# Performance work log

Measured on AMD Instinct MI355X. Metric: run time of the kernel, lower is better.

Reference implementation:

```python
import jax, jax.numpy as jnp
import numpy as np

B, C, L = 32, 64, 4096
HIDDEN = 64
SR = 50.0
KS = (7, 15, 31, 63)
PHYS = 12
EPS_BN = 1e-5
EPS_GN = 1e-5


def _dwconv(x, w):
    # x: (B,C,L), w: (C,1,k) depthwise kernel, SAME padding for odd k
    k = w.shape[-1]
    p = (k - 1) // 2
    return jax.lax.conv_general_dilated(
        x, w, window_strides=(1,), padding=[(p, p)],
        dimension_numbers=('NCH', 'OIH', 'NCH'),
        feature_group_count=x.shape[1])


def _physics(x):
    b, c, l = x.shape
    svm = jnp.sqrt((x * x).sum(axis=1))                      # (B,L) channel norm
    svm_max = svm.max(axis=-1)
    svm_mean = svm.mean(axis=-1)
    svm_std = jnp.std(svm, axis=-1, ddof=1) + 1e-6           # torch.std is unbiased
    jerk = jnp.diff(x, axis=-1) * SR                         # (B,C,L-1)
    jerk_max = jnp.abs(jerk).max(axis=-1).mean(axis=-1)      # (B,)
    jerk_rate = jnp.diff(jerk, axis=-1) * SR
    jerk_rate_max = jnp.abs(jerk_rate).max(axis=-1).mean(axis=-1)
    sign_changes = (x[:, :, :-1] * x[:, :, 1:] < 0).astype(x.dtype)
    zcr = sign_changes.sum(axis=-1).mean(axis=-1) / l
    thr = (svm_mean + 2.0 * svm_std)[:, None]
    impact_duration = (svm > thr).astype(x.dtype).sum(axis=-1) / l
    hthr = (svm_mean + 3.0 * svm_std)[:, None]
    impact_ratio = (svm > hthr).astype(x.dtype).sum(axis=-1) / l
    free_fall = (svm < (svm_mean - svm_std)[:, None]).astype(x.dtype).sum(axis=-1) / l
    second_half = svm[:, l // 2:]
    post_stillness = jnp.tanh(1.0 / (jnp.std(second_half, axis=-1, ddof=1) + 1e-6))
    third = max(1, l // 3)
    pre_mean = svm[:, :third].mean(axis=-1)
    impact_peak = svm[:, third:2 * third].max(axis=-1)
    post_mean = svm[:, 2 * third:].mean(axis=-1)
    fall_phase = jax.nn.relu(impact_peak - pre_mean) + jax.nn.relu(impact_peak - post_mean)
    fall_phase = fall_phase / (jnp.abs(impact_peak) + 1e-6)
    spectrum = jnp.fft.rfft(x.astype(jnp.float32), axis=-1, norm='ortho')
    power = (jnp.abs(spectrum) ** 2).sum(axis=1)             # (B, L//2+1)
    freqs = jnp.linspace(0.0, 1.0, power.shape[-1], dtype=power.dtype)
    total_power = power.sum(axis=-1) + 1e-6
    spectral_centroid = (power * freqs).sum(axis=-1) / total_power
    high_freq_ratio = jnp.where(freqs > 0.4, power, 0.0).sum(axis=-1) / total_power
    feats = jnp.stack([svm_max, svm_mean, jerk_max, jerk_rate_max, zcr,
                       impact_duration, impact_ratio, post_stillness, free_fall,
                       spectral_centroid, high_freq_ratio, fall_phase], axis=-1)
    return jnp.nan_to_num(feats, nan=0.0, posinf=0.0, neginf=0.0).astype(x.dtype)


def _forward(x, dw_w7, dw_w15, dw_w31, dw_w63, bn_g, bn_b, bn_m, bn_v,
             comp_w1, comp_b1, comp_w2, comp_b2,
             pn_g, pn_b, pn_m, pn_v,
             pe_w1, pe_b1, pe_w2, pe_b2, pg_w, pg_b,
             temperature, gn_g, gn_b, proj_w, proj_b, res_scale):
    # 4 depthwise conv + BN(eval) branches
    branches = []
    for i, w in enumerate((dw_w7, dw_w15, dw_w31, dw_w63)):
        y = _dwconv(x, w)
        y = (y - bn_m[i][None, :, None]) / jnp.sqrt(bn_v[i][None, :, None] + EPS_BN) \
            * bn_g[i][None, :, None] + bn_b[i][None, :, None]
        branches.append(y)
    stacked = jnp.stack(branches, axis=1)                    # (B,4,C,L)
    # complexity net: global avg pool -> MLP
    xm = x.mean(axis=-1)                                     # (B,C)
    h = jax.nn.relu(xm @ comp_w1 + comp_b1)
    complexity_logits = h @ comp_w2 + comp_b2                # (B,4)
    # physics gate
    pf = _physics(x)                                         # (B,12)
    pf = (pf - pn_m) / jnp.sqrt(pn_v + EPS_BN) * pn_g + pn_b
    pe = jax.nn.relu(jax.nn.relu(pf @ pe_w1 + pe_b1) @ pe_w2 + pe_b2)
    physics_weights = jax.nn.sigmoid(pe @ pg_w + pg_b)       # (B,4)
    temp = jnp.maximum(temperature, 0.1)
    weights = jax.nn.softmax(complexity_logits * physics_weights / temp, axis=-1)
    mixed = jnp.einsum('bkcl,bk->bcl', stacked, weights)
    # proj: GroupNorm(1,C) -> GELU(exact) -> 1x1 conv
    mu = mixed.mean(axis=(1, 2), keepdims=True)
    var = mixed.var(axis=(1, 2), keepdims=True)
    gn = (mixed - mu) / jnp.sqrt(var + EPS_GN) * gn_g[None, :, None] + gn_b[None, :, None]
    act = jax.nn.gelu(gn, approximate=False)
    out = jnp.einsum('oc,bcl->bol', proj_w, act) + proj_b[None, :, None]
    return x + res_scale * out


def setup_inputs() -> dict:
    ks = jax.random.split(jax.random.key(0), 16)
    f32 = jnp.float32
    inp = {}
    inp['x'] = jax.random.normal(ks[0], (B, C, L), dtype=f32)
    for i, k in enumerate(KS):
        inp[f'dw_w{k}'] = jax.random.normal(ks[1 + i], (C, 1, k), dtype=f32) / np.sqrt(k)
    inp['bn_g'] = jnp.ones((4, C), f32)
    inp['bn_b'] = jnp.zeros((4, C), f32)
    inp['bn_m'] = 0.1 * jax.random.normal(ks[5], (4, C), dtype=f32)
    inp['bn_v'] = jax.random.uniform(ks[6], (4, C), dtype=f32, minval=0.5, maxval=1.5)
    inp['comp_w1'] = jax.random.normal(ks[7], (C, HIDDEN), dtype=f32) / np.sqrt(C)
    inp['comp_b1'] = jnp.zeros((HIDDEN,), f32)
    inp['comp_w2'] = jax.random.normal(ks[8], (HIDDEN, 4), dtype=f32) / np.sqrt(HIDDEN)
    inp['comp_b2'] = jnp.zeros((4,), f32)
    inp['pn_g'] = jnp.ones((PHYS,), f32)
    inp['pn_b'] = jnp.zeros((PHYS,), f32)
    inp['pn_m'] = 0.1 * jax.random.normal(ks[9], (PHYS,), dtype=f32)
    inp['pn_v'] = jax.random.uniform(ks[10], (PHYS,), dtype=f32, minval=0.5, maxval=1.5)
    inp['pe_w1'] = jax.random.normal(ks[11], (PHYS, 32), dtype=f32) / np.sqrt(PHYS)
    inp['pe_b1'] = jnp.zeros((32,), f32)
    inp['pe_w2'] = jax.random.normal(ks[12], (32, 32), dtype=f32) / np.sqrt(32)
    inp['pe_b2'] = jnp.zeros((32,), f32)
    inp['pg_w'] = jax.random.normal(ks[13], (32, 4), dtype=f32) / np.sqrt(32)
    inp['pg_b'] = jnp.zeros((4,), f32)
    inp['temperature'] = jnp.asarray(1.0, f32)
    inp['gn_g'] = jnp.ones((C,), f32)
    inp['gn_b'] = jnp.zeros((C,), f32)
    inp['proj_w'] = jax.random.normal(ks[14], (C, C), dtype=f32) / np.sqrt(C)
    inp['proj_b'] = jnp.zeros((C,), f32)
    inp['res_scale'] = jnp.asarray(0.5, f32)  # init is 0.0; 0.5 gives a non-trivial output
    return inp


def reference(x, dw_w7, dw_w15, dw_w31, dw_w63, bn_g, bn_b, bn_m, bn_v,
              comp_w1, comp_b1, comp_w2, comp_b2,
              pn_g, pn_b, pn_m, pn_v,
              pe_w1, pe_b1, pe_w2, pe_b2, pg_w, pg_b,
              temperature, gn_g, gn_b, proj_w, proj_b, res_scale):
    return _forward(x, dw_w7, dw_w15, dw_w31, dw_w63, bn_g, bn_b, bn_m, bn_v,
                    comp_w1, comp_b1, comp_w2, comp_b2, pn_g, pn_b, pn_m, pn_v,
                    pe_w1, pe_b1, pe_w2, pe_b2, pg_w, pg_b,
                    temperature, gn_g, gn_b, proj_w, proj_b, res_scale)
```

## Files before the change

kernel.cpp:

```cpp
#include <hip/hip_runtime.h>
#include <math.h>

#define LN 4096
#define CN 64
#define BQ 32
#define NTH 256

#define OFF_CHAN_SUM    0
#define OFF_CHAN_JERK   2048
#define OFF_CHAN_JRATE  4096
#define OFF_CHAN_ZCR    6144
#define OFF_SVMST_PART  8192
#define OFF_SPEC_PART   12288
#define OFF_EFF_B       15360
#define OFF_GNP         17408
#define OFF_EFF_W       21504
#define OFF_SVMBUF      152576

#define FP(i) ((i) + ((i) >> 4))

__global__ __launch_bounds__(NTH) void kS(const float* __restrict__ x, float* __restrict__ ws) {
  __shared__ __align__(16) char smraw[34880];
  int role = blockIdx.x;
  int t = threadIdx.x;

  if (role < 2048) {
    int bc = role;
    const float* row = x + (size_t)bc * LN;
    int l0 = t * 16;
    float rd[18];
    const float4* r4 = (const float4*)(row + l0);
#pragma unroll
    for (int q = 0; q < 4; q++) {
      float4 v = r4[q];
      rd[4*q] = v.x; rd[4*q+1] = v.y; rd[4*q+2] = v.z; rd[4*q+3] = v.w;
    }
    if (t < 255) { rd[16] = row[l0 + 16]; rd[17] = row[l0 + 17]; }
    else { rd[16] = 0.f; rd[17] = 0.f; }
    float lsum = 0.f, jm = 0.f, jrm = 0.f; int zc = 0;
#pragma unroll
    for (int i = 0; i < 16; i++) {
      float a = rd[i], b2 = rd[i+1];
      lsum += a;
      int l = l0 + i;
      if (l < LN - 1) {
        jm = fmaxf(jm, fabsf(b2 - a));
        zc += (a * b2 < 0.f);
        if (l < LN - 2) jrm = fmaxf(jrm, fabsf(rd[i+2] - 2.f*b2 + a));
      }
    }
    for (int off = 32; off > 0; off >>= 1) {
      lsum += __shfl_down(lsum, off);
      jm = fmaxf(jm, __shfl_down(jm, off));
      jrm = fmaxf(jrm, __shfl_down(jrm, off));
      zc += __shfl_down(zc, off);
    }
    float* s1 = (float*)smraw; float* s2_ = s1 + 4; float* s3 = s1 + 8; int* s4 = (int*)(s1 + 12);
    int w = t >> 6;
    if ((t & 63) == 0) { s1[w] = lsum; s2_[w] = jm; s3[w] = jrm; s4[w] = zc; }
    __syncthreads();
    if (t == 0) {
      float S = 0, J = 0, JR = 0; int Z = 0;
      for (int i = 0; i < 4; i++) { S += s1[i]; J = fmaxf(J, s2_[i]); JR = fmaxf(JR, s3[i]); Z += s4[i]; }
      ws[OFF_CHAN_SUM + bc]   = S;
      ws[OFF_CHAN_JERK + bc]  = J * 50.f;
      ws[OFF_CHAN_JRATE + bc] = JR * 2500.f;
      ws[OFF_CHAN_ZCR + bc]   = (float)Z;
    }
  } else if (role < 2560) {
    int blk = role - 2048;
    int b = blk >> 4, lt = blk & 15;
    int l = lt * 256 + t;
    const float* xb = x + (size_t)b * CN * LN + l;
    float acc = 0.f;
#pragma unroll
    for (int c = 0; c < CN; c++) { float v = xb[(size_t)c * LN]; acc = fmaf(v, v, acc); }
    float svm = sqrtf(acc);
    ws[OFF_SVMBUF + (size_t)b * LN + l] = svm;
    const int third = LN / 3;
    float vS = svm, vS2 = svm * svm;
    float vS2H  = (l >= LN/2) ? svm : 0.f;
    float vS2H2 = (l >= LN/2) ? svm * svm : 0.f;
    float vPRE  = (l < third) ? svm : 0.f;
    float vPOST = (l >= 2*third) ? svm : 0.f;
    float vMX = svm;
    float vMID = (l >= third && l < 2*third) ? svm : 0.f;
    for (int off = 32; off > 0; off >>= 1) {
      vS += __shfl_down(vS, off); vS2 += __shfl_down(vS2, off);
      vS2H += __shfl_down(vS2H, off); vS2H2 += __shfl_down(vS2H2, off);
      vPRE += __shfl_down(vPRE, off); vPOST += __shfl_down(vPOST, off);
      vMX = fmaxf(vMX, __shfl_down(vMX, off));
      vMID = fmaxf(vMID, __shfl_down(vMID, off));
    }
    float (*red)[4] = (float(*)[4])smraw;
    int w = t >> 6;
    if ((t & 63) == 0) {
      red[0][w] = vS; red[1][w] = vS2; red[2][w] = vMX; red[3][w] = vS2H;
      red[4][w] = vS2H2; red[5][w] = vPRE; red[6][w] = vMID; red[7][w] = vPOST;
    }
    __syncthreads();
    if (t == 0) {
      float* sp = ws + OFF_SVMST_PART + (size_t)blk * 8;
      sp[0] = red[0][0]+red[0][1]+red[0][2]+red[0][3];
      sp[1] = red[1][0]+red[1][1]+red[1][2]+red[1][3];
      sp[2] = fmaxf(fmaxf(red[2][0],red[2][1]),fmaxf(red[2][2],red[2][3]));
      sp[3] = red[3][0]+red[3][1]+red[3][2]+red[3][3];
      sp[4] = red[4][0]+red[4][1]+red[4][2]+red[4][3];
      sp[5] = red[5][0]+red[5][1]+red[5][2]+red[5][3];
      sp[6] = fmaxf(fmaxf(red[6][0],red[6][1]),fmaxf(red[6][2],red[6][3]));
      sp[7] = red[7][0]+red[7][1]+red[7][2]+red[7][3];
    }
  } else {
    int blk = role - 2560;
    int b = blk >> 5, cp = blk & 31;
    const float* r0 = x + ((size_t)b * CN + 2 * cp) * LN;
    const float* r1 = r0 + LN;
    float2* z = (float2*)smraw;
    float (*red)[4] = (float(*)[4])(smraw + 34816);
#pragma unroll
    for (int k = 0; k < 4; k++) {
      int n4 = (k * 256 + t) * 4;
      float4 a = *(const float4*)(r0 + n4);
      float4 c = *(const float4*)(r1 + n4);
      float ar[4] = {a.x, a.y, a.z, a.w}, cr[4] = {c.x, c.y, c.z, c.w};
#pragma unroll
      for (int q = 0; q < 4; q++) {
        unsigned n = (unsigned)(n4 + q);
        unsigned br = __brev(n) >> 20;
        unsigned dr = ((br & 0x555u) << 1) | ((br & 0xAAAu) >> 1);
        z[FP(dr)] = make_float2(ar[q], cr[q]);
      }
    }
    __syncthreads();
#pragma unroll
    for (int u = 0; u < 4; u++) {
      int j = u * 256 + t;
      int i0 = 4 * j;
      float2 x0 = z[FP(i0)], x1 = z[FP(i0+1)], x2 = z[FP(i0+2)], x3 = z[FP(i0+3)];
      float ar = x0.x + x2.x, ai = x0.y + x2.y;
      float br_ = x0.x - x2.x, bi = x0.y - x2.y;
      float cr = x1.x + x3.x, ci = x1.y + x3.y;
      float dr_ = x1.x - x3.x, di = x1.y - x3.y;
      z[FP(i0)]   = make_float2(ar + cr, ai + ci);
      z[FP(i0+1)] = make_float2(br_ + di, bi - dr_);
      z[FP(i0+2)] = make_float2(ar - cr, ai - ci);
      z[FP(i0+3)] = make_float2(br_ - di, bi + dr_);
    }
    __syncthreads();
#pragma unroll
    for (int s = 1; s < 6; s++) {
      int half = 1 << (2 * s);
      float angscale = 1.0f / (float)(2 * half);
#pragma unroll
      for (int u = 0; u < 4; u++) {
        int j = u * 256 + t;
        int pos = j & (half - 1);
        int i0 = ((j >> (2 * s)) << (2 * s + 2)) + pos;
        float2 x0 = z[FP(i0)];
        float2 x1 = z[FP(i0 + half)];
        float2 x2 = z[FP(i0 + 2 * half)];
        float2 x3 = z[FP(i0 + 3 * half)];
        float sv, cv;
        sincospif((float)pos * angscale, &sv, &cv);
        float w1r = cv, w1i = -sv;
        float w2r = w1r*w1r - w1i*w1i, w2i = 2.f*w1r*w1i;
        float w3r = w2r*w1r - w2i*w1i, w3i = w2r*w1i + w2i*w1r;
        float t1r = x1.x*w1r - x1.y*w1i, t1i = x1.x*w1i + x1.y*w1r;
        float t2r = x2.x*w2r - x2.y*w2i, t2i = x2.x*w2i + x2.y*w2r;
        float t3r = x3.x*w3r - x3.y*w3i, t3i = x3.x*w3i + x3.y*w3r;
        float ar = x0.x + t2r, ai = x0.y + t2i;
        float br_ = x0.x - t2r, bi = x0.y - t2i;
        float cr = t1r + t3r, ci = t1i + t3i;
        float dr_ = t1r - t3r, di = t1i - t3i;
        z[FP(i0)]            = make_float2(ar + cr, ai + ci);
        z[FP(i0 + half)]     = make_float2(br_ + di, bi - dr_);
        z[FP(i0 + 2*half)]   = make_float2(ar - cr, ai - ci);
        z[FP(i0 + 3*half)]   = make_float2(br_ - di, bi + dr_);
      }
      __syncthreads();
    }
    float tot = 0.f, cen = 0.f, hi = 0.f;
    for (int k = t; k <= LN / 2; k += NTH) {
      float p;
      if (k == 0 || k == LN / 2) {
        float2 v = z[FP(k)];
        p = v.x * v.x + v.y * v.y;
      } else {
        float2 zk = z[FP(k)], zn = z[FP(LN - k)];
        float a1 = zk.x + zn.x, a2 = zk.y - zn.y, a3 = zk.y + zn.y, a4 = zk.x - zn.x;
        p = 0.25f * (a1*a1 + a2*a2 + a3*a3 + a4*a4);
      }
      p *= (1.0f / LN);
      tot += p;
      cen += p * ((float)k * (1.0f / (LN / 2)));
      if (k >= 820) hi += p;
    }
    for (int off = 32; off > 0; off >>= 1) {
      tot += __shfl_down(tot, off);
      cen += __shfl_down(cen, off);
      hi  += __shfl_down(hi, off);
    }
    int w = t >> 6;
    if ((t & 63) == 0) { red[0][w] = tot; red[1][w] = cen; red[2][w] = hi; }
    __syncthreads();
    if (t == 0) {
      float* sp = ws + OFF_SPEC_PART + (size_t)blk * 3;
      sp[0] = red[0][0]+red[0][1]+red[0][2]+red[0][3];
      sp[1] = red[1][0]+red[1][1]+red[1][2]+red[1][3];
      sp[2] = red[2][0]+red[2][1]+red[2][2]+red[2][3];
    }
  }
}

__global__ __launch_bounds__(NTH) void k4_gate(
    const float* __restrict__ dw7, const float* __restrict__ dw15,
    const float* __restrict__ dw31, const float* __restrict__ dw63,
    const float* __restrict__ bn_g, const float* __restrict__ bn_b,
    const float* __restrict__ bn_m, const float* __restrict__ bn_v,
    const float* __restrict__ comp_w1, const float* __restrict__ comp_b1,
    const float* __restrict__ comp_w2, const float* __restrict__ comp_b2,
    const float* __restrict__ pn_g, const float* __restrict__ pn_b,
    const float* __restrict__ pn_m, const float* __restrict__ pn_v,
    const float* __restrict__ pe_w1, const float* __restrict__ pe_b1,
    const float* __restrict__ pe_w2, const float* __restrict__ pe_b2,
    const float* __restrict__ pg_w, const float* __restrict__ pg_b,
    const float* __restrict__ temperature,
    float* __restrict__ ws)
{
  int b = blockIdx.x, t = threadIdx.x;
  __shared__ float sp8[16][8];
  __shared__ float sp3[32][3];
  __shared__ float stv[10];
  __shared__ float bc2[2];
  __shared__ float xm[64], h[64], pf[12], pe1v[32], pe2v[32], lgts[4], wts[4];
  __shared__ int ri[3][4], cnts[3];
  if (t < 16) {
    const float* p = ws + OFF_SVMST_PART + (size_t)(b * 16 + t) * 8;
#pragma unroll
    for (int i = 0; i < 8; i++) sp8[t][i] = p[i];
  }
  if (t >= 32 && t < 64) {
    int i = t - 32;
    const float* p = ws + OFF_SPEC_PART + (size_t)(b * 32 + i) * 3;
    sp3[i][0] = p[0]; sp3[i][1] = p[1]; sp3[i][2] = p[2];
  }
  __syncthreads();
  if (t == 0) {
    float S=0,S2=0,MX=-1e30f,S2H=0,S2H2=0,PRE=0,MID=-1e30f,POST=0;
    for (int i = 0; i < 16; i++) {
      S += sp8[i][0]; S2 += sp8[i][1]; MX = fmaxf(MX, sp8[i][2]);
      S2H += sp8[i][3]; S2H2 += sp8[i][4]; PRE += sp8[i][5];
      MID = fmaxf(MID, sp8[i][6]); POST += sp8[i][7];
    }
    float tot=0,cen=0,hi=0;
    for (int i = 0; i < 32; i++) { tot += sp3[i][0]; cen += sp3[i][1]; hi += sp3[i][2]; }
    stv[0]=S; stv[1]=S2; stv[2]=MX; stv[3]=S2H; stv[4]=S2H2;
    stv[5]=PRE; stv[6]=MID; stv[7]=POST; stv[8]=cen/(tot+1e-6f); stv[9]=hi/(tot+1e-6f);
    float mean = S * (1.f / LN);
    float var = (S2 - S * S * (1.f / LN)) * (1.f / (LN - 1));
    var = fmaxf(var, 0.f);
    bc2[0] = mean;
    bc2[1] = sqrtf(var) + 1e-6f;
  }
  __syncthreads();
  float mean = bc2[0], stde = bc2[1];
  float thr2 = mean + 2.f * stde, thr3 = mean + 3.f * stde, thrf = mean - stde;
  const float* svm = ws + OFF_SVMBUF + (size_t)b * LN;
  int c2 = 0, c3 = 0, cf = 0;
  for (int l = t; l < LN; l += NTH) {
    float v = svm[l];
    c2 += (v > thr2); c3 += (v > thr3); cf += (v < thrf);
  }
  for (int off = 32; off > 0; off >>= 1) {
    c2 += __shfl_down(c2, off); c3 += __shfl_down(c3, off); cf += __shfl_down(cf, off);
  }
  int w = t >> 6;
  if ((t & 63) == 0) { ri[0][w] = c2; ri[1][w] = c3; ri[2][w] = cf; }
  float j = 0.f, jr = 0.f, zz = 0.f;
  if (t < 64) {
    xm[t] = ws[OFF_CHAN_SUM + b * 64 + t] * (1.0f / LN);
    j  = ws[OFF_CHAN_JERK + b * 64 + t];
    jr = ws[OFF_CHAN_JRATE + b * 64 + t];
    zz = ws[OFF_CHAN_ZCR + b * 64 + t];
    for (int off = 32; off > 0; off >>= 1) {
      j += __shfl_down(j, off); jr += __shfl_down(jr, off); zz += __shfl_down(zz, off);
    }
  }
  __syncthreads();
  if (t == 0) {
    cnts[0] = ri[0][0]+ri[0][1]+ri[0][2]+ri[0][3];
    cnts[1] = ri[1][0]+ri[1][1]+ri[1][2]+ri[1][3];
    cnts[2] = ri[2][0]+ri[2][1]+ri[2][2]+ri[2][3];
    const int third = LN / 3;
    float S2H = stv[3], S2H2 = stv[4];
    float n2 = (float)(LN / 2);
    float var2 = (S2H2 - S2H * S2H / n2) / (n2 - 1.f);
    var2 = fmaxf(var2, 0.f);
    float post_still = tanhf(1.f / (sqrtf(var2) + 1e-6f));
    float pre_mean = stv[5] / (float)third;
    float post_mean = stv[7] / (float)(LN - 2 * third);
    float pk = stv[6];
    float fp = fmaxf(pk - pre_mean, 0.f) + fmaxf(pk - post_mean, 0.f);
    fp = fp / (fabsf(pk) + 1e-6f);
    pf[0] = stv[2];
    pf[1] = mean;
    pf[2] = j * (1.f / 64);
    pf[3] = jr * (1.f / 64);
    pf[4] = (zz * (1.f / 64)) * (1.f / LN);
    pf[5] = (float)cnts[0] / LN;
    pf[6] = (float)cnts[1] / LN;
    pf[7] = post_still;
    pf[8] = (float)cnts[2] / LN;
    pf[9] = stv[8];
    pf[10] = stv[9];
    pf[11] = fp;
  }
  __syncthreads();
  if (t < 12) pf[t] = (pf[t] - pn_m[t]) * rsqrtf(pn_v[t] + 1e-5f) * pn_g[t] + pn_b[t];
  __syncthreads();
  if (t < 64) {
    float hv = comp_b1[t];
    for (int i = 0; i < 64; i++) hv = fmaf(xm[i], comp_w1[i * 64 + t], hv);
    h[t] = fmaxf(hv, 0.f);
  }
  if (t < 32) {
    float v = pe_b1[t];
    for (int i = 0; i < 12; i++) v = fmaf(pf[i], pe_w1[i * 32 + t], v);
    pe1v[t] = fmaxf(v, 0.f);
  }
  __syncthreads();
  if (t < 32) {
    float v = pe_b2[t];
    for (int i = 0; i < 32; i++) v = fmaf(pe1v[i], pe_w2[i * 32 + t], v);
    pe2v[t] = fmaxf(v, 0.f);
  }
  __syncthreads();
  if (t < 4) {
    float v = comp_b2[t];
    for (int i = 0; i < 64; i++) v = fmaf(h[i], comp_w2[i * 4 + t], v);
    float g = pg_b[t];
    for (int i = 0; i < 32; i++) g = fmaf(pe2v[i], pg_w[i * 4 + t], g);
    g = 1.f / (1.f + expf(-g));
    float temp = fmaxf(temperature[0], 0.1f);
    lgts[t] = v * g / temp;
  }
  __syncthreads();
  if (t < 4) {
    float m = fmaxf(fmaxf(lgts[0], lgts[1]), fmaxf(lgts[2], lgts[3]));
    float den = expf(lgts[0]-m) + expf(lgts[1]-m) + expf(lgts[2]-m) + expf(lgts[3]-m);
    wts[t] = expf(lgts[t] - m) / den;
  }
  __syncthreads();
  if (t < 64) {
    int c = t;
    float w0 = wts[0], w1 = wts[1], w2 = wts[2], w3 = wts[3];
    float sc0 = bn_g[0*64+c] * rsqrtf(bn_v[0*64+c] + 1e-5f);
    float sc1 = bn_g[1*64+c] * rsqrtf(bn_v[1*64+c] + 1e-5f);
    float sc2 = bn_g[2*64+c] * rsqrtf(bn_v[2*64+c] + 1e-5f);
    float sc3 = bn_g[3*64+c] * rsqrtf(bn_v[3*64+c] + 1e-5f);
    float o0 = bn_b[0*64+c] - bn_m[0*64+c] * sc0;
    float o1 = bn_b[1*64+c] - bn_m[1*64+c] * sc1;
    float o2 = bn_b[2*64+c] - bn_m[2*64+c] * sc2;
    float o3 = bn_b[3*64+c] - bn_m[3*64+c] * sc3;
    ws[OFF_EFF_B + b * 64 + c] = w0*o0 + w1*o1 + w2*o2 + w3*o3;
    float a0 = w0*sc0, a1 = w1*sc1, a2 = w2*sc2, a3 = w3*sc3;
    float* eff = ws + OFF_EFF_W + (size_t)(b * 64 + c) * 64;
    for (int tau = 0; tau < 64; tau++) {
      float v = 0.f;
      if (tau < 63) {
        v = a3 * dw63[c * 63 + tau];
        int i7 = tau - 28;  if (i7 >= 0 && i7 < 7)   v = fmaf(a0, dw7[c * 7 + i7], v);
        int i15 = tau - 24; if (i15 >= 0 && i15 < 15) v = fmaf(a1, dw15[c * 15 + i15], v);
        int i31 = tau - 16; if (i31 >= 0 && i31 < 31) v = fmaf(a2, dw31[c * 31 + i31], v);
      }
      eff[tau] = v;
    }
  }
}

__device__ __forceinline__ float4 ldmask(const float* __restrict__ row, int idx) {
  int idxc = idx < 0 ? 0 : (idx > LN - 4 ? LN - 4 : idx);
  float4 v = *(const float4*)(row + idxc);
  float m = (idx == idxc) ? 1.f : 0.f;
  v.x *= m; v.y *= m; v.z *= m; v.w *= m;
  return v;
}

#define F16(wv,a0,a1,a2,a3,a4,a5,a6,a7,a8,a9,aA,aB,aC,aD,aE,aF) \
  acc[0]=fmaf(wv,a0,acc[0]);  acc[1]=fmaf(wv,a1,acc[1]);  acc[2]=fmaf(wv,a2,acc[2]);  acc[3]=fmaf(wv,a3,acc[3]);  \
  acc[4]=fmaf(wv,a4,acc[4]);  acc[5]=fmaf(wv,a5,acc[5]);  acc[6]=fmaf(wv,a6,acc[6]);  acc[7]=fmaf(wv,a7,acc[7]);  \
  acc[8]=fmaf(wv,a8,acc[8]);  acc[9]=fmaf(wv,a9,acc[9]);  acc[10]=fmaf(wv,aA,acc[10]); acc[11]=fmaf(wv,aB,acc[11]); \
  acc[12]=fmaf(wv,aC,acc[12]); acc[13]=fmaf(wv,aD,acc[13]); acc[14]=fmaf(wv,aE,acc[14]); acc[15]=fmaf(wv,aF,acc[15]);

__global__ __launch_bounds__(NTH) void k5_conv(const float* __restrict__ x,
                                               float* __restrict__ ws,
                                               float* __restrict__ mixed_out) {
  int bc = blockIdx.x;
  int t = threadIdx.x;
  __shared__ float wt[64];
  __shared__ float biasS;
  __shared__ double rda[2][4];
  if (t < 64) wt[t] = ws[OFF_EFF_W + (size_t)bc * 64 + t];
  if (t == 0) biasS = ws[OFF_EFF_B + bc];
  const float* row = x + (size_t)bc * LN;
  int l0 = t * 16;
  int g0 = l0 - 32;
  float4 R0 = ldmask(row, g0);
  float4 R1 = ldmask(row, g0 + 4);
  float4 R2 = ldmask(row, g0 + 8);
  float4 R3 = ldmask(row, g0 + 12);
  float4 R4 = ldmask(row, g0 + 16);
  __syncthreads();
  float bias = biasS;
  float acc[16];
#pragma unroll
  for (int jj = 0; jj < 16; jj++) acc[jj] = bias;
#pragma unroll
  for (int g = 0; g < 16; g++) {
    float w0 = wt[4*g], w1 = wt[4*g+1], w2 = wt[4*g+2], w3 = wt[4*g+3];
    F16(w0, R0.y,R0.z,R0.w,R1.x,R1.y,R1.z,R1.w,R2.x,R2.y,R2.z,R2.w,R3.x,R3.y,R3.z,R3.w,R4.x)
    F16(w1, R0.z,R0.w,R1.x,R1.y,R1.z,R1.w,R2.x,R2.y,R2.z,R2.w,R3.x,R3.y,R3.z,R3.w,R4.x,R4.y)
    F16(w2, R0.w,R1.x,R1.y,R1.z,R1.w,R2.x,R2.y,R2.z,R2.w,R3.x,R3.y,R3.z,R3.w,R4.x,R4.y,R4.z)
    F16(w3, R1.x,R1.y,R1.z,R1.w,R2.x,R2.y,R2.z,R2.w,R3.x,R3.y,R3.z,R3.w,R4.x,R4.y,R4.z,R4.w)
    if (g < 15) {
      R0 = R1; R1 = R2; R2 = R3; R3 = R4;
      R4 = ldmask(row, g0 + 4 * (g + 5));
    }
  }
  double ls = 0, ls2 = 0;
#pragma unroll
  for (int jj = 0; jj < 16; jj++) { float v = acc[jj]; ls += v; ls2 += (double)v * (double)v; }
  for (int off = 32; off > 0; off >>= 1) {
    ls += __shfl_down(ls, off);
    ls2 += __shfl_down(ls2, off);
  }
  int w = t >> 6;
  if ((t & 63) == 0) { rda[0][w] = ls; rda[1][w] = ls2; }
  __syncthreads();
  if (t == 0) {
    double* gp = (double*)(ws + OFF_GNP);
    gp[2 * bc + 0] = rda[0][0]+rda[0][1]+rda[0][2]+rda[0][3];
    gp[2 * bc + 1] = rda[1][0]+rda[1][1]+rda[1][2]+rda[1][3];
  }
  float* dst = mixed_out + (size_t)bc * LN + l0;
#pragma unroll
  for (int q = 0; q < 4; q++) {
    float4 v; v.x = acc[4*q]; v.y = acc[4*q+1]; v.z = acc[4*q+2]; v.w = acc[4*q+3];
    *(float4*)(dst + 4 * q) = v;
  }
}

__global__ __launch_bounds__(NTH) void k6_final(const float* __restrict__ x,
    const float* __restrict__ proj_w, const float* __restrict__ proj_b,
    const float* __restrict__ gn_g, const float* __restrict__ gn_b,
    const float* __restrict__ res_scale,
    const float* __restrict__ ws, float* out) {
  int blk = blockIdx.x;
  int b = blk >> 5;
  int l0 = (blk & 31) * 128;
  __shared__ float actS[64 * 128];
  __shared__ float Wt[64 * 64];
  __shared__ double rg[2][4];
  __shared__ float bcst[2];
  int t = threadIdx.x;
  {
    const double* gp = (const double*)(ws + OFF_GNP) + (size_t)b * CN * 2;
    double s1 = 0, s2 = 0;
    for (int i = t; i < CN; i += NTH) { s1 += gp[2*i]; s2 += gp[2*i+1]; }
    for (int off = 32; off > 0; off >>= 1) { s1 += __shfl_down(s1, off); s2 += __shfl_down(s2, off); }
    int w = t >> 6;
    if ((t & 63) == 0) { rg[0][w] = s1; rg[1][w] = s2; }
    __syncthreads();
    if (t == 0) {
      double S1 = rg[0][0]+rg[0][1]+rg[0][2]+rg[0][3];
      double S2 = rg[1][0]+rg[1][1]+rg[1][2]+rg[1][3];
      const double NN = 64.0 * 4096.0;
      double mud = S1 / NN;
      bcst[0] = (float)mud;
      bcst[1] = rsqrtf((float)(S2 / NN - mud * mud) + 1e-5f);
    }
  }
  for (int i = t; i < 4096; i += NTH) {
    int o = i & 63, c = i >> 6;
    Wt[c * 64 + o] = proj_w[o * 64 + c];
  }
  __syncthreads();
  float mu = bcst[0], rstd = bcst[1];
  const float* mx = out + (size_t)b * CN * LN;
  for (int i = t; i < 8192; i += NTH) {
    int c = i >> 7, l = i & 127;
    float v = mx[(size_t)c * LN + l0 + l];
    float g = (v - mu) * rstd * gn_g[c] + gn_b[c];
    float a = 0.5f * g * (1.f + erff(g * 0.70710678118654752f));
    actS[c * 128 + l] = a;
  }
  __syncthreads();
  int lg = t & 31;
  int og = (t >> 5) * 8;
  float4 acc4[8];
#pragma unroll
  for (int q = 0; q < 8; q++) { acc4[q].x = 0.f; acc4[q].y = 0.f; acc4[q].z = 0.f; acc4[q].w = 0.f; }
  for (int c = 0; c < 64; c++) {
    float4 a = *(const float4*)&actS[c * 128 + lg * 4];
    float4 wlo = *(const float4*)&Wt[c * 64 + og];
    float4 whi = *(const float4*)&Wt[c * 64 + og + 4];
    float wv[8] = { wlo.x, wlo.y, wlo.z, wlo.w, whi.x, whi.y, whi.z, whi.w };
#pragma unroll
    for (int q = 0; q < 8; q++) {
      acc4[q].x = fmaf(wv[q], a.x, acc4[q].x);
      acc4[q].y = fmaf(wv[q], a.y, acc4[q].y);
      acc4[q].z = fmaf(wv[q], a.z, acc4[q].z);
      acc4[q].w = fmaf(wv[q], a.w, acc4[q].w);
    }
  }
  float rsv = res_scale[0];
  const float* xb = x + (size_t)b * CN * LN;
  float* ob = out + (size_t)b * CN * LN;
#pragma unroll
  for (int q = 0; q < 8; q++) {
    int o = og + q;
    float pb = proj_b[o];
    size_t base = (size_t)o * LN + l0 + lg * 4;
    float4 xv = *(const float4*)&xb[base];
    float4 r;
    r.x = xv.x + rsv * (acc4[q].x + pb);
    r.y = xv.y + rsv * (acc4[q].y + pb);
    r.z = xv.z + rsv * (acc4[q].z + pb);
    r.w = xv.w + rsv * (acc4[q].w + pb);
    *(float4*)&ob[base] = r;
  }
}

extern "C" void kernel_launch(void* const* d_in, const int* in_sizes, int n_in,
                              void* d_out, int out_size, void* d_ws, size_t ws_size,
                              hipStream_t stream) {
  const float* x        = (const float*)d_in[0];
  const float* dw7      = (const float*)d_in[1];
  const float* dw15     = (const float*)d_in[2];
  const float* dw31     = (const float*)d_in[3];
  const float* dw63     = (const float*)d_in[4];
  const float* bn_g     = (const float*)d_in[5];
  const float* bn_b     = (const float*)d_in[6];
  const float* bn_m     = (const float*)d_in[7];
  const float* bn_v     = (const float*)d_in[8];
  const float* comp_w1  = (const float*)d_in[9];
  const float* comp_b1  = (const float*)d_in[10];
  const float* comp_w2  = (const float*)d_in[11];
  const float* comp_b2  = (const float*)d_in[12];
  const float* pn_g     = (const float*)d_in[13];
  const float* pn_b     = (const float*)d_in[14];
  const float* pn_m     = (const float*)d_in[15];
  const float* pn_v     = (const float*)d_in[16];
  const float* pe_w1    = (const float*)d_in[17];
  const float* pe_b1    = (const float*)d_in[18];
  const float* pe_w2    = (const float*)d_in[19];
  const float* pe_b2    = (const float*)d_in[20];
  const float* pg_w     = (const float*)d_in[21];
  const float* pg_b     = (const float*)d_in[22];
  const float* temperature = (const float*)d_in[23];
  const float* gn_g     = (const float*)d_in[24];
  const float* gn_b     = (const float*)d_in[25];
  const float* proj_w   = (const float*)d_in[26];
  const float* proj_b   = (const float*)d_in[27];
  const float* res_scale= (const float*)d_in[28];
  float* ws = (float*)d_ws;
  float* out = (float*)d_out;

  hipLaunchKernelGGL(kS, dim3(2048 + 512 + 1024), dim3(NTH), 0, stream, x, ws);
  hipLaunchKernelGGL(k4_gate, dim3(BQ), dim3(NTH), 0, stream,
                     dw7, dw15, dw31, dw63, bn_g, bn_b, bn_m, bn_v,
                     comp_w1, comp_b1, comp_w2, comp_b2,
                     pn_g, pn_b, pn_m, pn_v, pe_w1, pe_b1, pe_w2, pe_b2,
                     pg_w, pg_b, temperature, ws);
  hipLaunchKernelGGL(k5_conv, dim3(BQ * CN), dim3(NTH), 0, stream, x, ws, out);
  hipLaunchKernelGGL(k6_final, dim3(BQ * 32), dim3(NTH), 0, stream,
                     x, proj_w, proj_b, gn_g, gn_b, res_scale, ws, out);
}
```

Baseline: 242.2 us.

## Fuse radix-4 FFT stages into radix-16 register passes

Replaces the six radix-4 FFT stages over shared memory with three passes. In each pass a thread loads 16 elements into registers and applies two radix-4 layers there. This halves the number of shared-memory round trips and barriers in the spectrum computation. The cost is higher register pressure and twiddles built from chained products, which may lose some accuracy.

```diff
diff --git a/kernel.cpp b/kernel.cpp
--- a/kernel.cpp
+++ b/kernel.cpp
@@ -18,6 +18,22 @@
 #define OFF_SVMBUF      152576
 
 #define FP(i) ((i) + ((i) >> 4))
+
+__device__ __forceinline__ void bfly4(float2& a, float2& b, float2& c, float2& d,
+                                      float w1r, float w1i, float w2r, float w2i,
+                                      float w3r, float w3i) {
+  float t1r = b.x*w1r - b.y*w1i, t1i = b.x*w1i + b.y*w1r;
+  float t2r = c.x*w2r - c.y*w2i, t2i = c.x*w2i + c.y*w2r;
+  float t3r = d.x*w3r - d.y*w3i, t3i = d.x*w3i + d.y*w3r;
+  float ar = a.x + t2r, ai = a.y + t2i;
+  float br = a.x - t2r, bi = a.y - t2i;
+  float cr = t1r + t3r, ci = t1i + t3i;
+  float dr = t1r - t3r, di = t1i - t3i;
+  a = make_float2(ar + cr, ai + ci);
+  b = make_float2(br + di, bi - dr);
+  c = make_float2(ar - cr, ai - ci);
+  d = make_float2(br - di, bi + dr);
+}
 
 __global__ __launch_bounds__(NTH) void kS(const float* __restrict__ x, float* __restrict__ ws) {
   __shared__ __align__(16) char smraw[34880];
@@ -132,51 +148,36 @@
       }
     }
     __syncthreads();
-#pragma unroll
-    for (int u = 0; u < 4; u++) {
-      int j = u * 256 + t;
-      int i0 = 4 * j;
-      float2 x0 = z[FP(i0)], x1 = z[FP(i0+1)], x2 = z[FP(i0+2)], x3 = z[FP(i0+3)];
-      float ar = x0.x + x2.x, ai = x0.y + x2.y;
-      float br_ = x0.x - x2.x, bi = x0.y - x2.y;
-      float cr = x1.x + x3.x, ci = x1.y + x3.y;
-      float dr_ = x1.x - x3.x, di = x1.y - x3.y;
-      z[FP(i0)]   = make_float2(ar + cr, ai + ci);
-      z[FP(i0+1)] = make_float2(br_ + di, bi - dr_);
-      z[FP(i0+2)] = make_float2(ar - cr, ai - ci);
-      z[FP(i0+3)] = make_float2(br_ - di, bi + dr_);
-    }
-    __syncthreads();
-#pragma unroll
-    for (int s = 1; s < 6; s++) {
-      int half = 1 << (2 * s);
-      float angscale = 1.0f / (float)(2 * half);
-#pragma unroll
-      for (int u = 0; u < 4; u++) {
-        int j = u * 256 + t;
-        int pos = j & (half - 1);
-        int i0 = ((j >> (2 * s)) << (2 * s + 2)) + pos;
-        float2 x0 = z[FP(i0)];
-        float2 x1 = z[FP(i0 + half)];
-        float2 x2 = z[FP(i0 + 2 * half)];
-        float2 x3 = z[FP(i0 + 3 * half)];
-        float sv, cv;
-        sincospif((float)pos * angscale, &sv, &cv);
-        float w1r = cv, w1i = -sv;
-        float w2r = w1r*w1r - w1i*w1i, w2i = 2.f*w1r*w1i;
-        float w3r = w2r*w1r - w2i*w1i, w3i = w2r*w1i + w2i*w1r;
-        float t1r = x1.x*w1r - x1.y*w1i, t1i = x1.x*w1i + x1.y*w1r;
-        float t2r = x2.x*w2r - x2.y*w2i, t2i = x2.x*w2i + x2.y*w2r;
-        float t3r = x3.x*w3r - x3.y*w3i, t3i = x3.x*w3i + x3.y*w3r;
-        float ar = x0.x + t2r, ai = x0.y + t2i;
-        float br_ = x0.x - t2r, bi = x0.y - t2i;
-        float cr = t1r + t3r, ci = t1i + t3i;
-        float dr_ = t1r - t3r, di = t1i - t3i;
-        z[FP(i0)]            = make_float2(ar + cr, ai + ci);
-        z[FP(i0 + half)]     = make_float2(br_ + di, bi - dr_);
-        z[FP(i0 + 2*half)]   = make_float2(ar - cr, ai - ci);
-        z[FP(i0 + 3*half)]   = make_float2(br_ - di, bi + dr_);
+    const float c8r[4] = { 1.f, 0.92387953251f, 0.70710678119f, 0.38268343236f };
+    const float c8i[4] = { 0.f, -0.38268343236f, -0.70710678119f, -0.92387953251f };
+#pragma unroll
+    for (int p = 0; p < 3; p++) {
+      const int H = (p == 0) ? 1 : (p == 1) ? 16 : 256;
+      int r = t & (H - 1);
+      int B = ((t / H) * 16 * H) + r;
+      float2 E[16];
+#pragma unroll
+      for (int q = 0; q < 16; q++) E[q] = z[FP(B + q * H)];
+      float su, cu;
+      sincospif((float)r / (8.0f * (float)H), &su, &cu);
+      float ur = cu, ui = -su;
+      float u2r = ur*ur - ui*ui, u2i = 2.f*ur*ui;
+      float w1r = u2r*u2r - u2i*u2i, w1i = 2.f*u2r*u2i;
+      float w2r = w1r*w1r - w1i*w1i, w2i = 2.f*w1r*w1i;
+      float w3r = w2r*w1r - w2i*w1i, w3i = w2r*w1i + w2i*w1r;
+#pragma unroll
+      for (int m = 0; m < 4; m++)
+        bfly4(E[4*m], E[4*m+1], E[4*m+2], E[4*m+3], w1r, w1i, w2r, w2i, w3r, w3i);
+#pragma unroll
+      for (int m = 0; m < 4; m++) {
+        float W1r = ur*c8r[m] - ui*c8i[m];
+        float W1i = ur*c8i[m] + ui*c8r[m];
+        float W2r = W1r*W1r - W1i*W1i, W2i = 2.f*W1r*W1i;
+        float W3r = W2r*W1r - W2i*W1i, W3i = W2r*W1i + W2i*W1r;
+        bfly4(E[m], E[m+4], E[m+8], E[m+12], W1r, W1i, W2r, W2i, W3r, W3i);
       }
+#pragma unroll
+      for (int q = 0; q < 16; q++) z[FP(B + q * H)] = E[q];
       __syncthreads();
     }
     float tot = 0.f, cen = 0.f, hi = 0.f;
```

After: 240.7 us. Within noise of the previous version (-0.6%).
